# Performance work log

Hardware: AMD Instinct MI355X
Metric: run time of the kernel (lower is better)

The kernel has to match this reference:

```python
import jax, jax.numpy as jnp
import numpy as np

B, N = 2048, 4096

def setup_inputs() -> dict:
    key = jax.random.key(0)
    k1, k2, k3, k4, k5 = jax.random.split(key, 5)
    scale = 1.0 / np.sqrt(N)  # match nn.Linear init scale
    return {
        "t": jnp.zeros((1,), dtype=jnp.float32),
        "y": jax.random.uniform(k1, (B, N), dtype=jnp.float32),
        "W1": jax.random.normal(k2, (N, N), dtype=jnp.float32) * scale,
        "b1": jax.random.normal(k3, (N,), dtype=jnp.float32) * scale,
        "W2": jax.random.normal(k4, (N, N), dtype=jnp.float32) * scale,
        "b2": jax.random.normal(k5, (N,), dtype=jnp.float32) * scale,
    }

def reference(t, y, W1, b1, W2, b2):
    # out = fcc2(fcc1(y)) : two Linear layers (y @ W^T + b)
    h = y @ W1.T + b1            # [B, N]
    out = h @ W2.T + b2          # [B, N]
    # f = ones(N,1) @ y @ out^T  ==  dot(y, out) broadcast over N;
    # dydt = y * (out - dot(y, out))   (replicator equation)
    dot = jnp.sum(y * out, axis=-1, keepdims=True)  # [B, 1]
    return y * (out - dot)       # [B, N]
```

## Files before the change

kernel.cpp:

```cpp
#include <hip/hip_runtime.h>
#include <hip/hip_bf16.h>
#include <stdint.h>

typedef _Float16 f16;
typedef _Float16 f16x4 __attribute__((ext_vector_type(4)));
typedef _Float16 f16x8 __attribute__((ext_vector_type(8)));
typedef float f32x4 __attribute__((ext_vector_type(4)));

#define ASYNC_COPY16(gsrc, ldst)                                                   \
    __builtin_amdgcn_global_load_lds(                                              \
        (__attribute__((address_space(1))) void*)(gsrc),                           \
        (__attribute__((address_space(3))) void*)(ldst), 16, 0, 0)

__global__ __launch_bounds__(256) void cvt_f32_to_f16(const float* __restrict__ in,
                                                      f16* __restrict__ out, int n4) {
    int i = blockIdx.x * 256 + threadIdx.x;
    if (i >= n4) return;
    float4 v = ((const float4*)in)[i];
    f16x4 o;
    o.x = (f16)v.x; o.y = (f16)v.y; o.z = (f16)v.z; o.w = (f16)v.w;
    ((f16x4*)out)[i] = o;
}

template <int STORE_F16>
__global__ __launch_bounds__(256) void gemm_bt(const f16* __restrict__ A,
                                               const f16* __restrict__ Bm,
                                               const float* __restrict__ bias,
                                               void* __restrict__ Cout,
                                               int M, int N, int K) {
    constexpr int BM = 128, BN = 128, BK = 32;
    __shared__ __align__(16) f16 sA[BM * BK];
    __shared__ __align__(16) f16 sB[BN * BK];

    const int tid   = threadIdx.x;
    const int lane  = tid & 63;
    const int wave  = tid >> 6;
    const int waveM = wave >> 1;
    const int waveN = wave & 1;

    const int bm = blockIdx.y * BM;
    const int bn = blockIdx.x * BN;

    const int srow = lane >> 2;
    const int scol = (lane & 3) * 8;

    const f16* Aptr = A + (size_t)bm * K;
    const f16* Bptr = Bm + (size_t)bn * K;

    f32x4 acc[4][4] = {};

    const int quad = lane >> 4;
    const int l16  = lane & 15;

    for (int k0 = 0; k0 < K; k0 += BK) {
        {
            const int r0 = wave * 16 + srow;
            const int r1 = r0 + 64;
            ASYNC_COPY16(Aptr + (size_t)r0 * K + k0 + scol, &sA[r0 * BK + scol]);
            ASYNC_COPY16(Aptr + (size_t)r1 * K + k0 + scol, &sA[r1 * BK + scol]);
            ASYNC_COPY16(Bptr + (size_t)r0 * K + k0 + scol, &sB[r0 * BK + scol]);
            ASYNC_COPY16(Bptr + (size_t)r1 * K + k0 + scol, &sB[r1 * BK + scol]);
        }
        __syncthreads();

        f16x8 af[4], bf[4];
#pragma unroll
        for (int mi = 0; mi < 4; mi++)
            af[mi] = *(const f16x8*)&sA[(waveM * 64 + mi * 16 + l16) * BK + quad * 8];
#pragma unroll
        for (int ni = 0; ni < 4; ni++)
            bf[ni] = *(const f16x8*)&sB[(waveN * 64 + ni * 16 + l16) * BK + quad * 8];

#pragma unroll
        for (int mi = 0; mi < 4; mi++)
#pragma unroll
            for (int ni = 0; ni < 4; ni++)
                acc[mi][ni] = __builtin_amdgcn_mfma_f32_16x16x32_f16(af[mi], bf[ni],
                                                                     acc[mi][ni], 0, 0, 0);
        __syncthreads();
    }

#pragma unroll
    for (int ni = 0; ni < 4; ni++) {
        const int col = bn + waveN * 64 + ni * 16 + l16;
        const float bv = bias[col];
#pragma unroll
        for (int mi = 0; mi < 4; mi++) {
            const int row0 = bm + waveM * 64 + mi * 16 + quad * 4;
#pragma unroll
            for (int r = 0; r < 4; r++) {
                float v = acc[mi][ni][r] + bv;
                if (STORE_F16)
                    ((f16*)Cout)[(size_t)(row0 + r) * N + col] = (f16)v;
                else
                    ((float*)Cout)[(size_t)(row0 + r) * N + col] = v;
            }
        }
    }
}

__global__ __launch_bounds__(256) void replicator(const float* __restrict__ y,
                                                  float* __restrict__ out, int N) {
    const int row = blockIdx.x;
    const float4* y4 = (const float4*)(y + (size_t)row * N);
    float4* o4 = (float4*)(out + (size_t)row * N);
    const int n4 = N / 4;

    float p = 0.f;
    for (int i = threadIdx.x; i < n4; i += 256) {
        float4 a = y4[i], b = o4[i];
        p += a.x * b.x + a.y * b.y + a.z * b.z + a.w * b.w;
    }
#pragma unroll
    for (int off = 32; off > 0; off >>= 1) p += __shfl_down(p, off, 64);

    __shared__ float sred[4];
    if ((threadIdx.x & 63) == 0) sred[threadIdx.x >> 6] = p;
    __syncthreads();
    const float dot = sred[0] + sred[1] + sred[2] + sred[3];

    for (int i = threadIdx.x; i < n4; i += 256) {
        float4 a = y4[i], b = o4[i];
        float4 r;
        r.x = a.x * (b.x - dot);
        r.y = a.y * (b.y - dot);
        r.z = a.z * (b.z - dot);
        r.w = a.w * (b.w - dot);
        o4[i] = r;
    }
}

extern "C" void kernel_launch(void* const* d_in, const int* in_sizes, int n_in,
                              void* d_out, int out_size, void* d_ws, size_t ws_size,
                              hipStream_t stream) {
    const float* y  = (const float*)d_in[1];
    const float* W1 = (const float*)d_in[2];
    const float* b1 = (const float*)d_in[3];
    const float* W2 = (const float*)d_in[4];
    const float* b2 = (const float*)d_in[5];

    const int N = in_sizes[3];
    const int B = in_sizes[1] / N;
    float* out = (float*)d_out;

    f16* yb = (f16*)d_ws;
    f16* wb = yb + (size_t)B * N;
    f16* hb = wb + (size_t)N * N;

    const int yn4 = (B * N) / 4;
    const int wn4 = (N * N) / 4;

    cvt_f32_to_f16<<<yn4 / 256, 256, 0, stream>>>(y, yb, yn4);
    cvt_f32_to_f16<<<wn4 / 256, 256, 0, stream>>>(W1, wb, wn4);

    dim3 g1(N / 128, B / 128);
    gemm_bt<1><<<g1, 256, 0, stream>>>(yb, wb, b1, hb, B, N, N);

    cvt_f32_to_f16<<<wn4 / 256, 256, 0, stream>>>(W2, wb, wn4);

    gemm_bt<0><<<g1, 256, 0, stream>>>(hb, wb, b2, out, B, N, N);

    replicator<<<B, 256, 0, stream>>>(y, out, N);
}
```

Measured before the change: 409.6 us.

## Shrink GEMM tile to 128x64 with two waves and fuse the three f32-to-f16 conversions

The GEMM block shrinks from 256 threads with a 128x128 tile to 128 threads with a 128x64 tile. This doubles the grid to 64x16 blocks, which should fill the CUs better, but each block reuses less data from LDS. When the workspace is large enough, the y, W1 and W2 conversions are merged into one launch writing separate W1/W2 buffers, which removes two kernel launches. Each wave still computes a 64x64 sub-tile, so per-wave register and MFMA work is unchanged.

```diff
diff --git a/kernel.cpp b/kernel.cpp
--- a/kernel.cpp
+++ b/kernel.cpp
@@ -22,27 +22,50 @@
     ((f16x4*)out)[i] = o;
 }
 
+__global__ __launch_bounds__(256) void cvt3_f32_to_f16(const float* __restrict__ y,
+                                                       const float* __restrict__ W1,
+                                                       const float* __restrict__ W2,
+                                                       f16* __restrict__ yb,
+                                                       f16* __restrict__ w1b,
+                                                       f16* __restrict__ w2b,
+                                                       int nY4, int nW4) {
+    int i = blockIdx.x * 256 + threadIdx.x;
+    const float* src;
+    f16* dst;
+    int off;
+    if (i < nY4) {
+        src = y; dst = yb; off = i;
+    } else if (i < nY4 + nW4) {
+        src = W1; dst = w1b; off = i - nY4;
+    } else {
+        src = W2; dst = w2b; off = i - nY4 - nW4;
+        if (off >= nW4) return;
+    }
+    float4 v = ((const float4*)src)[off];
+    f16x4 o;
+    o.x = (f16)v.x; o.y = (f16)v.y; o.z = (f16)v.z; o.w = (f16)v.w;
+    ((f16x4*)dst)[off] = o;
+}
+
 template <int STORE_F16>
-__global__ __launch_bounds__(256) void gemm_bt(const f16* __restrict__ A,
+__global__ __launch_bounds__(128) void gemm_bt(const f16* __restrict__ A,
                                                const f16* __restrict__ Bm,
                                                const float* __restrict__ bias,
                                                void* __restrict__ Cout,
                                                int M, int N, int K) {
-    constexpr int BM = 128, BN = 128, BK = 32;
+    constexpr int BM = 128, BN = 64, BK = 32;
     __shared__ __align__(16) f16 sA[BM * BK];
     __shared__ __align__(16) f16 sB[BN * BK];
 
-    const int tid   = threadIdx.x;
-    const int lane  = tid & 63;
-    const int wave  = tid >> 6;
-    const int waveM = wave >> 1;
-    const int waveN = wave & 1;
+    const int tid  = threadIdx.x;
+    const int lane = tid & 63;
+    const int wave = tid >> 6;
 
     const int bm = blockIdx.y * BM;
     const int bn = blockIdx.x * BN;
 
-    const int srow = lane >> 2;
-    const int scol = (lane & 3) * 8;
+    const int srow = tid >> 2;
+    const int scol = (tid & 3) * 8;
 
     const f16* Aptr = A + (size_t)bm * K;
     const f16* Bptr = Bm + (size_t)bn * K;
@@ -53,23 +76,25 @@
     const int l16  = lane & 15;
 
     for (int k0 = 0; k0 < K; k0 += BK) {
-        {
-            const int r0 = wave * 16 + srow;
-            const int r1 = r0 + 64;
-            ASYNC_COPY16(Aptr + (size_t)r0 * K + k0 + scol, &sA[r0 * BK + scol]);
-            ASYNC_COPY16(Aptr + (size_t)r1 * K + k0 + scol, &sA[r1 * BK + scol]);
-            ASYNC_COPY16(Bptr + (size_t)r0 * K + k0 + scol, &sB[r0 * BK + scol]);
-            ASYNC_COPY16(Bptr + (size_t)r1 * K + k0 + scol, &sB[r1 * BK + scol]);
+#pragma unroll
+        for (int i = 0; i < 4; i++) {
+            const int r = srow + 32 * i;
+            ASYNC_COPY16(Aptr + (size_t)r * K + k0 + scol, &sA[r * BK + scol]);
+        }
+#pragma unroll
+        for (int j = 0; j < 2; j++) {
+            const int r = srow + 32 * j;
+            ASYNC_COPY16(Bptr + (size_t)r * K + k0 + scol, &sB[r * BK + scol]);
         }
         __syncthreads();
 
         f16x8 af[4], bf[4];
 #pragma unroll
         for (int mi = 0; mi < 4; mi++)
-            af[mi] = *(const f16x8*)&sA[(waveM * 64 + mi * 16 + l16) * BK + quad * 8];
+            af[mi] = *(const f16x8*)&sA[(wave * 64 + mi * 16 + l16) * BK + quad * 8];
 #pragma unroll
         for (int ni = 0; ni < 4; ni++)
-            bf[ni] = *(const f16x8*)&sB[(waveN * 64 + ni * 16 + l16) * BK + quad * 8];
+            bf[ni] = *(const f16x8*)&sB[(ni * 16 + l16) * BK + quad * 8];
 
 #pragma unroll
         for (int mi = 0; mi < 4; mi++)
@@ -82,11 +107,11 @@
 
 #pragma unroll
     for (int ni = 0; ni < 4; ni++) {
-        const int col = bn + waveN * 64 + ni * 16 + l16;
+        const int col = bn + ni * 16 + l16;
         const float bv = bias[col];
 #pragma unroll
         for (int mi = 0; mi < 4; mi++) {
-            const int row0 = bm + waveM * 64 + mi * 16 + quad * 4;
+            const int row0 = bm + wave * 64 + mi * 16 + quad * 4;
 #pragma unroll
             for (int r = 0; r < 4; r++) {
                 float v = acc[mi][ni][r] + bv;
@@ -143,22 +168,38 @@
     const int B = in_sizes[1] / N;
     float* out = (float*)d_out;
 
-    f16* yb = (f16*)d_ws;
-    f16* wb = yb + (size_t)B * N;
-    f16* hb = wb + (size_t)N * N;
-
-    const int yn4 = (B * N) / 4;
-    const int wn4 = (N * N) / 4;
-
-    cvt_f32_to_f16<<<yn4 / 256, 256, 0, stream>>>(y, yb, yn4);
-    cvt_f32_to_f16<<<wn4 / 256, 256, 0, stream>>>(W1, wb, wn4);
-
-    dim3 g1(N / 128, B / 128);
-    gemm_bt<1><<<g1, 256, 0, stream>>>(yb, wb, b1, hb, B, N, N);
-
-    cvt_f32_to_f16<<<wn4 / 256, 256, 0, stream>>>(W2, wb, wn4);
-
-    gemm_bt<0><<<g1, 256, 0, stream>>>(hb, wb, b2, out, B, N, N);
+    const size_t szY = (size_t)B * N;
+    const size_t szW = (size_t)N * N;
+
+    const int yn4 = (int)(szY / 4);
+    const int wn4 = (int)(szW / 4);
+
+    dim3 g1(N / 64, B / 128);
+
+    const size_t need_big = (szY + 2 * szW + szY) * sizeof(f16);
+
+    if (ws_size >= need_big) {
+        f16* yb  = (f16*)d_ws;
+        f16* w1b = yb + szY;
+        f16* w2b = w1b + szW;
+        f16* hb  = w2b + szW;
+
+        const int tot4 = yn4 + 2 * wn4;
+        cvt3_f32_to_f16<<<(tot4 + 255) / 256, 256, 0, stream>>>(y, W1, W2, yb, w1b, w2b,
+                                                                yn4, wn4);
+        gemm_bt<1><<<g1, 128, 0, stream>>>(yb, w1b, b1, hb, B, N, N);
+        gemm_bt<0><<<g1, 128, 0, stream>>>(hb, w2b, b2, out, B, N, N);
+    } else {
+        f16* yb = (f16*)d_ws;
+        f16* wb = yb + szY;
+        f16* hb = wb + szW;
+
+        cvt_f32_to_f16<<<yn4 / 256, 256, 0, stream>>>(y, yb, yn4);
+        cvt_f32_to_f16<<<wn4 / 256, 256, 0, stream>>>(W1, wb, wn4);
+        gemm_bt<1><<<g1, 128, 0, stream>>>(yb, wb, b1, hb, B, N, N);
+        cvt_f32_to_f16<<<wn4 / 256, 256, 0, stream>>>(W2, wb, wn4);
+        gemm_bt<0><<<g1, 128, 0, stream>>>(hb, wb, b2, out, B, N, N);
+    }
 
     replicator<<<B, 256, 0, stream>>>(y, out, N);
 }
```

Result: slower. 433.3 us (+5.8%).
